# Performance work log

Hardware: AMD Instinct MI355X
Metric: run time of the kernel (lower is better)

Reference implementation:

```python
import jax, jax.numpy as jnp
import numpy as np

N_AUTHORS = 50000
N_PAPERS = 100000
N_NODES = N_AUTHORS + N_PAPERS
N_EDGES = 1200000
EMB_DIM = 64
NUM_LAYERS = 3


def setup_inputs() -> dict:
    key = jax.random.key(0)
    k1, k2, k3, k4, k5 = jax.random.split(key, 5)
    author_embedding = jax.random.normal(k1, (N_AUTHORS, EMB_DIM), dtype=jnp.float32)
    paper_embedding = jax.random.normal(k2, (N_PAPERS, EMB_DIM), dtype=jnp.float32)
    adj_rows = jax.random.randint(k3, (N_EDGES,), 0, N_NODES, dtype=jnp.int32)
    adj_cols = jax.random.randint(k4, (N_EDGES,), 0, N_NODES, dtype=jnp.int32)
    # symmetric-normalized adjacency values are small positive floats
    adj_vals = jax.random.uniform(k5, (N_EDGES,), dtype=jnp.float32) * 0.1
    return {
        "author_embedding": author_embedding,
        "paper_embedding": paper_embedding,
        "adj_rows": adj_rows,
        "adj_cols": adj_cols,
        "adj_vals": adj_vals,
    }


def _spmm(adj_rows, adj_cols, adj_vals, x):
    # sparse [N,N] @ dense [N,d] via gather + segment_sum
    msgs = adj_vals[:, None] * x[adj_cols]  # [E, d]
    return jax.ops.segment_sum(msgs, adj_rows, num_segments=N_NODES)


def reference(author_embedding, paper_embedding, adj_rows, adj_cols, adj_vals):
    ego = jnp.concatenate([author_embedding, paper_embedding], axis=0)  # [N, d]
    acc = ego
    x = ego
    for _ in range(NUM_LAYERS):
        x = _spmm(adj_rows, adj_cols, adj_vals, x)
        acc = acc + x
    out = acc / jnp.float32(NUM_LAYERS + 1)  # mean over layer outputs
    out_author = out[:N_AUTHORS]
    out_paper = out[N_AUTHORS:]
    return ego, out_author, out_paper
```

## Files before the change

kernel.cpp:

```cpp
#include <hip/hip_runtime.h>

#define N_AUTHORS 50000
#define N_PAPERS  100000
#define N_NODES   150000
#define N_EDGES   1200000
#define EMB       64

#define BSHIFT 10
#define K_B    ((N_NODES + 1023) >> 10)
#define CHUNK  4096
#define NBLK_A ((N_EDGES + CHUNK - 1) / CHUNK)
#define NSC    (K_B * NBLK_A)
#define NBS1   ((NSC + 1023) / 1024)

typedef float v2f __attribute__((ext_vector_type(2)));

__device__ __forceinline__ ushort f2bf(float f) {
    unsigned u = __float_as_uint(f);
    return (ushort)((u + 0x7fffu + ((u >> 16) & 1u)) >> 16);
}
#define bfLO(u) __uint_as_float((u) << 16)
#define bfHI(u) __uint_as_float((u) & 0xffff0000u)

__device__ __forceinline__ v2f mkv2(float a, float b) { v2f r; r.x = a; r.y = b; return r; }
__device__ __forceinline__ v2f bfv2(unsigned u) { return mkv2(bfLO(u), bfHI(u)); }

__device__ __forceinline__ v2f red_v2(v2f v) {
#pragma unroll
    for (int s = 8; s <= 32; s <<= 1) {
        v2f o;
        o.x = __shfl_xor(v.x, s, 64);
        o.y = __shfl_xor(v.y, s, 64);
        v += o;
    }
    return v;
}

__global__ void lgcn_hist_init(const int* __restrict__ rows,
                               unsigned* __restrict__ counts,
                               const float* __restrict__ a,
                               const float* __restrict__ p,
                               float* __restrict__ ego_out,
                               ushort* __restrict__ x0) {
    __shared__ unsigned h[K_B];
    int t = threadIdx.x;
    if (blockIdx.x < NBLK_A) {
        for (int i = t; i < K_B; i += blockDim.x) h[i] = 0;
        __syncthreads();
        int base = blockIdx.x * CHUNK;
        int end  = base + CHUNK; if (end > N_EDGES) end = N_EDGES;
        for (int e = base + t; e < end; e += blockDim.x)
            atomicAdd(&h[rows[e] >> BSHIFT], 1u);
        __syncthreads();
        for (int i = t; i < K_B; i += blockDim.x)
            counts[(size_t)i * NBLK_A + blockIdx.x] = h[i];
    } else {
        size_t i = (size_t)(blockIdx.x - NBLK_A) * blockDim.x + t;
        const size_t n4  = (size_t)N_NODES  * EMB / 4;
        const size_t au4 = (size_t)N_AUTHORS * EMB / 4;
        if (i >= n4) return;
        float4 v = (i < au4) ? ((const float4*)a)[i] : ((const float4*)p)[i - au4];
        ((float4*)ego_out)[i] = v;
        ushort4 b;
        b.x = f2bf(v.x); b.y = f2bf(v.y); b.z = f2bf(v.z); b.w = f2bf(v.w);
        ((ushort4*)x0)[i] = b;
    }
}

__global__ void lgcn_scan_l1(const unsigned* __restrict__ counts,
                             unsigned* __restrict__ scanned,
                             unsigned* __restrict__ btot) {
    __shared__ unsigned s[1024];
    int t = threadIdx.x;
    int i = blockIdx.x * 1024 + t;
    unsigned v = (i < NSC) ? counts[i] : 0u;
    s[t] = v;
    __syncthreads();
    for (int d = 1; d < 1024; d <<= 1) {
        unsigned u = (t >= d) ? s[t - d] : 0u;
        __syncthreads();
        s[t] += u;
        __syncthreads();
    }
    if (i < NSC) scanned[i] = s[t] - v;
    if (t == 1023) btot[blockIdx.x] = s[1023];
}

__device__ __forceinline__ void btot_prefix(const unsigned* __restrict__ btot,
                                            unsigned* __restrict__ btex) {
    if (threadIdx.x == 0) {
        unsigned run = 0;
        for (int i = 0; i < NBS1; ++i) { btex[i] = run; run += btot[i]; }
    }
    __syncthreads();
}

__global__ void lgcn_a1_bin(const int* __restrict__ rows,
                            const int* __restrict__ cols,
                            const float* __restrict__ vals,
                            const unsigned* __restrict__ scanned,
                            const unsigned* __restrict__ btot,
                            float2* __restrict__ stage) {
    __shared__ unsigned cur[K_B];
    __shared__ unsigned btex[NBS1];
    btot_prefix(btot, btex);
    int t = threadIdx.x;
    for (int i = t; i < K_B; i += blockDim.x) {
        unsigned idx = (unsigned)i * NBLK_A + blockIdx.x;
        cur[i] = scanned[idx] + btex[idx >> 10];
    }
    __syncthreads();
    int base = blockIdx.x * CHUNK;
    int end  = base + CHUNK; if (end > N_EDGES) end = N_EDGES;
    for (int e = base + t; e < end; e += blockDim.x) {
        int r = rows[e];
        unsigned pos = atomicAdd(&cur[r >> BSHIFT], 1u);
        unsigned packed = ((unsigned)(r & 1023) << 18) | (unsigned)cols[e];
        stage[pos] = make_float2(__uint_as_float(packed), vals[e]);
    }
}

__global__ void lgcn_place(const unsigned* __restrict__ scanned,
                           const unsigned* __restrict__ btot,
                           const float2* __restrict__ stage,
                           float2* __restrict__ se,
                           unsigned* __restrict__ row_start) {
    __shared__ unsigned cur[1 << BSHIFT];
    __shared__ unsigned tsum[256];
    __shared__ unsigned btex[NBS1];
    btot_prefix(btot, btex);
    int b  = blockIdx.x;
    int rb = b << BSHIFT;
    int nrows = N_NODES - rb; if (nrows > (1 << BSHIFT)) nrows = 1 << BSHIFT;
    int t = threadIdx.x;

    unsigned i0 = (unsigned)b * NBLK_A;
    unsigned base = scanned[i0] + btex[i0 >> 10];
    unsigned span1;
    if (b + 1 < K_B) {
        unsigned i1 = (unsigned)(b + 1) * NBLK_A;
        span1 = scanned[i1] + btex[i1 >> 10];
    } else span1 = N_EDGES;

    for (int i = t; i < (1 << BSHIFT); i += 256) cur[i] = 0;
    __syncthreads();
    for (unsigned p = base + t; p < span1; p += 256)
        atomicAdd(&cur[__float_as_uint(stage[p].x) >> 18], 1u);
    __syncthreads();

    unsigned c[4], s = 0;
#pragma unroll
    for (int k = 0; k < 4; ++k) { c[k] = cur[t * 4 + k]; s += c[k]; }
    tsum[t] = s;
    __syncthreads();
    for (int d = 1; d < 256; d <<= 1) {
        unsigned u = (t >= d) ? tsum[t - d] : 0u;
        __syncthreads();
        tsum[t] += u;
        __syncthreads();
    }
    unsigned run = base + (tsum[t] - s);
    __syncthreads();
#pragma unroll
    for (int k = 0; k < 4; ++k) {
        int i = t * 4 + k;
        cur[i] = run;
        if (i < nrows) row_start[rb + i] = run;
        run += c[k];
    }
    if (b == K_B - 1 && t == 0) row_start[N_NODES] = N_EDGES;
    __syncthreads();

    for (unsigned p = base + t; p < span1; p += 256) {
        float2 v = stage[p];
        unsigned u = __float_as_uint(v.x);
        unsigned pos = atomicAdd(&cur[u >> 18], 1u);
        se[pos] = make_float2(__int_as_float((int)(u & 0x3FFFFu)), v.y);
    }
}

template <int MODE>
__global__ void lgcn_spmm(const unsigned* __restrict__ rs,
                          const float2* __restrict__ se,
                          const ushort* __restrict__ xb,
                          const unsigned char* __restrict__ x8,
                          unsigned char* __restrict__ y8,
                          const ushort* __restrict__ egob,
                          const unsigned char* __restrict__ y18,
                          float* __restrict__ out) {
    int w    = blockIdx.x * (blockDim.x >> 6) + (threadIdx.x >> 6);
    int lane = threadIdx.x & 63;
    int r0   = w << 1;
    if (r0 >= N_NODES) return;
    unsigned jA   = rs[r0];
    unsigned endA = rs[r0 + 1];
    unsigned jB   = endA;
    unsigned endB = rs[r0 + 2];
    const int g  = lane >> 3;
    const int d8 = (lane & 7) << 3;
    v2f A0 = {0.f, 0.f}, A1 = A0, A2 = A0, A3 = A0;
    v2f B0 = A0, B1 = A0, B2 = A0, B3 = A0;

#define BATCH8(JB, END, P0, P1, P2, P3)                                       \
    {                                                                         \
        unsigned idx = (JB) + g;                                              \
        float2 e;                                                             \
        if (idx < (END)) e = se[idx];                                         \
        else { e.x = __int_as_float(0); e.y = 0.f; }                          \
        v2f ey = mkv2(e.y, e.y);                                              \
        if constexpr (MODE == 0) {                                            \
            const uint4 xv = *(const uint4*)(xb + ((size_t)__float_as_int(e.x) << 6) + d8); \
            P0 += ey * bfv2(xv.x);                                            \
            P1 += ey * bfv2(xv.y);                                            \
            P2 += ey * bfv2(xv.z);                                            \
            P3 += ey * bfv2(xv.w);                                            \
        } else {                                                              \
            const uint2 xv = *(const uint2*)(x8 + ((size_t)__float_as_int(e.x) << 6) + d8); \
            P0 += ey * __builtin_amdgcn_cvt_pk_f32_fp8((int)xv.x, false);     \
            P1 += ey * __builtin_amdgcn_cvt_pk_f32_fp8((int)xv.x, true);      \
            P2 += ey * __builtin_amdgcn_cvt_pk_f32_fp8((int)xv.y, false);     \
            P3 += ey * __builtin_amdgcn_cvt_pk_f32_fp8((int)xv.y, true);      \
        }                                                                     \
    }

    BATCH8(jA, endA, A0, A1, A2, A3)
    BATCH8(jB, endB, B0, B1, B2, B3)
    jA += 8; jB += 8;
    while (jA < endA) { BATCH8(jA, endA, A0, A1, A2, A3) jA += 8; }
    while (jB < endB) { BATCH8(jB, endB, B0, B1, B2, B3) jB += 8; }
#undef BATCH8

    A0 = red_v2(A0); A1 = red_v2(A1); A2 = red_v2(A2); A3 = red_v2(A3);
    B0 = red_v2(B0); B1 = red_v2(B1); B2 = red_v2(B2); B3 = red_v2(B3);

    if (g == 0) {
#define EMIT(ROW, P0, P1, P2, P3)                                             \
    {                                                                         \
        size_t o = ((size_t)(ROW) << 6) + d8;                                 \
        if constexpr (MODE == 2) {                                            \
            uint4 ue = *(const uint4*)(egob + o);                             \
            uint2 u1 = *(const uint2*)(y18 + o);                              \
            uint2 u2 = *(const uint2*)(x8 + o);                               \
            v2f q = mkv2(0.25f, 0.25f);                                       \
            v2f r0 = (bfv2(ue.x) + __builtin_amdgcn_cvt_pk_f32_fp8((int)u1.x, false) \
                      + __builtin_amdgcn_cvt_pk_f32_fp8((int)u2.x, false) + P0) * q; \
            v2f r1 = (bfv2(ue.y) + __builtin_amdgcn_cvt_pk_f32_fp8((int)u1.x, true)  \
                      + __builtin_amdgcn_cvt_pk_f32_fp8((int)u2.x, true) + P1) * q; \
            v2f r2 = (bfv2(ue.z) + __builtin_amdgcn_cvt_pk_f32_fp8((int)u1.y, false) \
                      + __builtin_amdgcn_cvt_pk_f32_fp8((int)u2.y, false) + P2) * q; \
            v2f r3 = (bfv2(ue.w) + __builtin_amdgcn_cvt_pk_f32_fp8((int)u1.y, true)  \
                      + __builtin_amdgcn_cvt_pk_f32_fp8((int)u2.y, true) + P3) * q; \
            float4 lo, hi;                                                    \
            lo.x = r0.x; lo.y = r0.y; lo.z = r1.x; lo.w = r1.y;               \
            hi.x = r2.x; hi.y = r2.y; hi.z = r3.x; hi.w = r3.y;               \
            *(float4*)(out + o)     = lo;                                     \
            *(float4*)(out + o + 4) = hi;                                     \
        } else {                                                              \
            int w0 = __builtin_amdgcn_cvt_pk_fp8_f32(P0.x, P0.y, 0, false);   \
            w0     = __builtin_amdgcn_cvt_pk_fp8_f32(P1.x, P1.y, w0, true);   \
            int w1 = __builtin_amdgcn_cvt_pk_fp8_f32(P2.x, P2.y, 0, false);   \
            w1     = __builtin_amdgcn_cvt_pk_fp8_f32(P3.x, P3.y, w1, true);   \
            uint2 ov8; ov8.x = (unsigned)w0; ov8.y = (unsigned)w1;            \
            *(uint2*)(y8 + o) = ov8;                                          \
        }                                                                     \
    }
        EMIT(r0, A0, A1, A2, A3)
        EMIT(r0 + 1, B0, B1, B2, B3)
#undef EMIT
    }
}

extern "C" void kernel_launch(void* const* d_in, const int* in_sizes, int n_in,
                              void* d_out, int out_size, void* d_ws, size_t ws_size,
                              hipStream_t stream) {
    const float* author = (const float*)d_in[0];
    const float* paper  = (const float*)d_in[1];
    const int*   rows   = (const int*)d_in[2];
    const int*   cols   = (const int*)d_in[3];
    const float* vals   = (const float*)d_in[4];

    float* ego_out = (float*)d_out;
    float* acc     = (float*)d_out + (size_t)N_NODES * EMB;

    char* w = (char*)d_ws;
    float2*   se        = (float2*)w;   w += (size_t)N_EDGES * sizeof(float2);
    float2*   stage     = (float2*)w;   w += (size_t)N_EDGES * sizeof(float2);
    ushort*   xbE       = (ushort*)w;   w += (size_t)N_NODES * EMB * sizeof(ushort);
    unsigned char* y2_8 = (unsigned char*)w; w += (size_t)N_NODES * EMB;
    unsigned* row_start = (unsigned*)w; w += (size_t)(N_NODES + 1) * 4;
    unsigned* bcounts   = (unsigned*)w; w += (size_t)NSC * 4;
    unsigned* bscanned  = (unsigned*)w; w += (size_t)NSC * 4;
    unsigned* btot      = (unsigned*)w; w += 64 * 4;
    unsigned char* y1_8 = (unsigned char*)stage;

    const int BLK = 256;
    const int g_vec  = (int)(((size_t)N_NODES * EMB / 4 + BLK - 1) / BLK);
    const int g_spmm = ((N_NODES / 2) + 3) / 4;

    lgcn_hist_init<<<NBLK_A + g_vec, BLK, 0, stream>>>(rows, bcounts,
                                                       author, paper, ego_out, xbE);

    lgcn_scan_l1<<<NBS1, 1024, 0, stream>>>(bcounts, bscanned, btot);

    lgcn_a1_bin<<<NBLK_A, BLK, 0, stream>>>(rows, cols, vals, bscanned, btot, stage);
    lgcn_place<<<K_B, BLK, 0, stream>>>(bscanned, btot, stage, se, row_start);

    lgcn_spmm<0><<<g_spmm, BLK, 0, stream>>>(row_start, se, xbE, nullptr,
                                             y1_8, nullptr, nullptr, nullptr);
    lgcn_spmm<1><<<g_spmm, BLK, 0, stream>>>(row_start, se, nullptr, y1_8,
                                             y2_8, nullptr, nullptr, nullptr);
    lgcn_spmm<2><<<g_spmm, BLK, 0, stream>>>(row_start, se, nullptr, y2_8,
                                             nullptr, xbE, y1_8, acc);
}
```

Measured before the change: 191.9 us.

## Split each SpMM layer into two column-range passes for gather locality

Each row's edges are now sorted into two halves by source column (below or above 75000), and row_mid marks the boundary. Each SpMM layer then runs as two passes, one per column half, so the gathered source features of each pass fit better in L2/MALL. The first pass writes a bf16 partial result that the second pass reads back and adds. This costs an extra launch per layer and an extra round trip of the partial buffer, and it adds one bf16 rounding step.

```diff
diff --git a/kernel.cpp b/kernel.cpp
--- a/kernel.cpp
+++ b/kernel.cpp
@@ -5,6 +5,7 @@
 #define N_NODES   150000
 #define N_EDGES   1200000
 #define EMB       64
+#define COL_SPLIT 75000u
 
 #define BSHIFT 10
 #define K_B    ((N_NODES + 1023) >> 10)
@@ -124,8 +125,9 @@
                            const unsigned* __restrict__ btot,
                            const float2* __restrict__ stage,
                            float2* __restrict__ se,
-                           unsigned* __restrict__ row_start) {
-    __shared__ unsigned cur[1 << BSHIFT];
+                           unsigned* __restrict__ row_start,
+                           unsigned* __restrict__ row_mid) {
+    __shared__ unsigned cur[2048];
     __shared__ unsigned tsum[256];
     __shared__ unsigned btex[NBS1];
     btot_prefix(btot, btex);
@@ -142,15 +144,18 @@
         span1 = scanned[i1] + btex[i1 >> 10];
     } else span1 = N_EDGES;
 
-    for (int i = t; i < (1 << BSHIFT); i += 256) cur[i] = 0;
-    __syncthreads();
-    for (unsigned p = base + t; p < span1; p += 256)
-        atomicAdd(&cur[__float_as_uint(stage[p].x) >> 18], 1u);
-    __syncthreads();
-
-    unsigned c[4], s = 0;
+    for (int i = t; i < 2048; i += 256) cur[i] = 0;
+    __syncthreads();
+    for (unsigned p = base + t; p < span1; p += 256) {
+        unsigned u = __float_as_uint(stage[p].x);
+        unsigned bin = ((u >> 18) << 1) | ((u & 0x3FFFFu) >= COL_SPLIT ? 1u : 0u);
+        atomicAdd(&cur[bin], 1u);
+    }
+    __syncthreads();
+
+    unsigned c[8], s = 0;
 #pragma unroll
-    for (int k = 0; k < 4; ++k) { c[k] = cur[t * 4 + k]; s += c[k]; }
+    for (int k = 0; k < 8; ++k) { c[k] = cur[t * 8 + k]; s += c[k]; }
     tsum[t] = s;
     __syncthreads();
     for (int d = 1; d < 256; d <<= 1) {
@@ -162,10 +167,14 @@
     unsigned run = base + (tsum[t] - s);
     __syncthreads();
 #pragma unroll
-    for (int k = 0; k < 4; ++k) {
-        int i = t * 4 + k;
-        cur[i] = run;
-        if (i < nrows) row_start[rb + i] = run;
+    for (int k = 0; k < 8; ++k) {
+        int bin = t * 8 + k;
+        cur[bin] = run;
+        int row = bin >> 1;
+        if (row < nrows) {
+            if ((bin & 1) == 0) row_start[rb + row] = run;
+            else                row_mid[rb + row]   = run;
+        }
         run += c[k];
     }
     if (b == K_B - 1 && t == 0) row_start[N_NODES] = N_EDGES;
@@ -174,16 +183,20 @@
     for (unsigned p = base + t; p < span1; p += 256) {
         float2 v = stage[p];
         unsigned u = __float_as_uint(v.x);
-        unsigned pos = atomicAdd(&cur[u >> 18], 1u);
-        se[pos] = make_float2(__int_as_float((int)(u & 0x3FFFFu)), v.y);
-    }
-}
-
-template <int MODE>
+        unsigned col = u & 0x3FFFFu;
+        unsigned bin = ((u >> 18) << 1) | (col >= COL_SPLIT ? 1u : 0u);
+        unsigned pos = atomicAdd(&cur[bin], 1u);
+        se[pos] = make_float2(__int_as_float((int)col), v.y);
+    }
+}
+
+template <int MODE, int PASS>
 __global__ void lgcn_spmm(const unsigned* __restrict__ rs,
+                          const unsigned* __restrict__ rmid,
                           const float2* __restrict__ se,
                           const ushort* __restrict__ xb,
                           const unsigned char* __restrict__ x8,
+                          ushort* __restrict__ yp,
                           unsigned char* __restrict__ y8,
                           const ushort* __restrict__ egob,
                           const unsigned char* __restrict__ y18,
@@ -192,10 +205,14 @@
     int lane = threadIdx.x & 63;
     int r0   = w << 1;
     if (r0 >= N_NODES) return;
-    unsigned jA   = rs[r0];
-    unsigned endA = rs[r0 + 1];
-    unsigned jB   = endA;
-    unsigned endB = rs[r0 + 2];
+    unsigned jA, endA, jB, endB;
+    if constexpr (PASS == 0) {
+        jA = rs[r0];       endA = rmid[r0];
+        jB = rs[r0 + 1];   endB = rmid[r0 + 1];
+    } else {
+        jA = rmid[r0];     endA = rs[r0 + 1];
+        jB = rmid[r0 + 1]; endB = rs[r0 + 2];
+    }
     const int g  = lane >> 3;
     const int d8 = (lane & 7) << 3;
     v2f A0 = {0.f, 0.f}, A1 = A0, A2 = A0, A3 = A0;
@@ -237,31 +254,43 @@
 #define EMIT(ROW, P0, P1, P2, P3)                                             \
     {                                                                         \
         size_t o = ((size_t)(ROW) << 6) + d8;                                 \
-        if constexpr (MODE == 2) {                                            \
-            uint4 ue = *(const uint4*)(egob + o);                             \
-            uint2 u1 = *(const uint2*)(y18 + o);                              \
-            uint2 u2 = *(const uint2*)(x8 + o);                               \
-            v2f q = mkv2(0.25f, 0.25f);                                       \
-            v2f r0 = (bfv2(ue.x) + __builtin_amdgcn_cvt_pk_f32_fp8((int)u1.x, false) \
-                      + __builtin_amdgcn_cvt_pk_f32_fp8((int)u2.x, false) + P0) * q; \
-            v2f r1 = (bfv2(ue.y) + __builtin_amdgcn_cvt_pk_f32_fp8((int)u1.x, true)  \
-                      + __builtin_amdgcn_cvt_pk_f32_fp8((int)u2.x, true) + P1) * q; \
-            v2f r2 = (bfv2(ue.z) + __builtin_amdgcn_cvt_pk_f32_fp8((int)u1.y, false) \
-                      + __builtin_amdgcn_cvt_pk_f32_fp8((int)u2.y, false) + P2) * q; \
-            v2f r3 = (bfv2(ue.w) + __builtin_amdgcn_cvt_pk_f32_fp8((int)u1.y, true)  \
-                      + __builtin_amdgcn_cvt_pk_f32_fp8((int)u2.y, true) + P3) * q; \
-            float4 lo, hi;                                                    \
-            lo.x = r0.x; lo.y = r0.y; lo.z = r1.x; lo.w = r1.y;               \
-            hi.x = r2.x; hi.y = r2.y; hi.z = r3.x; hi.w = r3.y;               \
-            *(float4*)(out + o)     = lo;                                     \
-            *(float4*)(out + o + 4) = hi;                                     \
+        if constexpr (PASS == 0) {                                            \
+            uint4 ov;                                                         \
+            ov.x = (unsigned)f2bf(P0.x) | ((unsigned)f2bf(P0.y) << 16);       \
+            ov.y = (unsigned)f2bf(P1.x) | ((unsigned)f2bf(P1.y) << 16);       \
+            ov.z = (unsigned)f2bf(P2.x) | ((unsigned)f2bf(P2.y) << 16);       \
+            ov.w = (unsigned)f2bf(P3.x) | ((unsigned)f2bf(P3.y) << 16);       \
+            *(uint4*)(yp + o) = ov;                                           \
         } else {                                                              \
-            int w0 = __builtin_amdgcn_cvt_pk_fp8_f32(P0.x, P0.y, 0, false);   \
-            w0     = __builtin_amdgcn_cvt_pk_fp8_f32(P1.x, P1.y, w0, true);   \
-            int w1 = __builtin_amdgcn_cvt_pk_fp8_f32(P2.x, P2.y, 0, false);   \
-            w1     = __builtin_amdgcn_cvt_pk_fp8_f32(P3.x, P3.y, w1, true);   \
-            uint2 ov8; ov8.x = (unsigned)w0; ov8.y = (unsigned)w1;            \
-            *(uint2*)(y8 + o) = ov8;                                          \
+            uint4 pv = *(const uint4*)(yp + o);                               \
+            P0 += bfv2(pv.x); P1 += bfv2(pv.y);                               \
+            P2 += bfv2(pv.z); P3 += bfv2(pv.w);                               \
+            if constexpr (MODE == 2) {                                        \
+                uint4 ue = *(const uint4*)(egob + o);                         \
+                uint2 u1 = *(const uint2*)(y18 + o);                          \
+                uint2 u2 = *(const uint2*)(x8 + o);                           \
+                v2f q = mkv2(0.25f, 0.25f);                                   \
+                v2f r0v = (bfv2(ue.x) + __builtin_amdgcn_cvt_pk_f32_fp8((int)u1.x, false) \
+                          + __builtin_amdgcn_cvt_pk_f32_fp8((int)u2.x, false) + P0) * q; \
+                v2f r1v = (bfv2(ue.y) + __builtin_amdgcn_cvt_pk_f32_fp8((int)u1.x, true)  \
+                          + __builtin_amdgcn_cvt_pk_f32_fp8((int)u2.x, true) + P1) * q; \
+                v2f r2v = (bfv2(ue.z) + __builtin_amdgcn_cvt_pk_f32_fp8((int)u1.y, false) \
+                          + __builtin_amdgcn_cvt_pk_f32_fp8((int)u2.y, false) + P2) * q; \
+                v2f r3v = (bfv2(ue.w) + __builtin_amdgcn_cvt_pk_f32_fp8((int)u1.y, true)  \
+                          + __builtin_amdgcn_cvt_pk_f32_fp8((int)u2.y, true) + P3) * q; \
+                float4 lo, hi;                                                \
+                lo.x = r0v.x; lo.y = r0v.y; lo.z = r1v.x; lo.w = r1v.y;       \
+                hi.x = r2v.x; hi.y = r2v.y; hi.z = r3v.x; hi.w = r3v.y;       \
+                *(float4*)(out + o)     = lo;                                 \
+                *(float4*)(out + o + 4) = hi;                                 \
+            } else {                                                          \
+                int w0 = __builtin_amdgcn_cvt_pk_fp8_f32(P0.x, P0.y, 0, false); \
+                w0     = __builtin_amdgcn_cvt_pk_fp8_f32(P1.x, P1.y, w0, true); \
+                int w1 = __builtin_amdgcn_cvt_pk_fp8_f32(P2.x, P2.y, 0, false); \
+                w1     = __builtin_amdgcn_cvt_pk_fp8_f32(P3.x, P3.y, w1, true); \
+                uint2 ov8; ov8.x = (unsigned)w0; ov8.y = (unsigned)w1;        \
+                *(uint2*)(y8 + o) = ov8;                                      \
+            }                                                                 \
         }                                                                     \
     }
         EMIT(r0, A0, A1, A2, A3)
@@ -286,8 +315,10 @@
     float2*   se        = (float2*)w;   w += (size_t)N_EDGES * sizeof(float2);
     float2*   stage     = (float2*)w;   w += (size_t)N_EDGES * sizeof(float2);
     ushort*   xbE       = (ushort*)w;   w += (size_t)N_NODES * EMB * sizeof(ushort);
+    ushort*   yp        = (ushort*)w;   w += (size_t)N_NODES * EMB * sizeof(ushort);
     unsigned char* y2_8 = (unsigned char*)w; w += (size_t)N_NODES * EMB;
     unsigned* row_start = (unsigned*)w; w += (size_t)(N_NODES + 1) * 4;
+    unsigned* row_mid   = (unsigned*)w; w += (size_t)N_NODES * 4;
     unsigned* bcounts   = (unsigned*)w; w += (size_t)NSC * 4;
     unsigned* bscanned  = (unsigned*)w; w += (size_t)NSC * 4;
     unsigned* btot      = (unsigned*)w; w += 64 * 4;
@@ -303,12 +334,18 @@
     lgcn_scan_l1<<<NBS1, 1024, 0, stream>>>(bcounts, bscanned, btot);
 
     lgcn_a1_bin<<<NBLK_A, BLK, 0, stream>>>(rows, cols, vals, bscanned, btot, stage);
-    lgcn_place<<<K_B, BLK, 0, stream>>>(bscanned, btot, stage, se, row_start);
-
-    lgcn_spmm<0><<<g_spmm, BLK, 0, stream>>>(row_start, se, xbE, nullptr,
-                                             y1_8, nullptr, nullptr, nullptr);
-    lgcn_spmm<1><<<g_spmm, BLK, 0, stream>>>(row_start, se, nullptr, y1_8,
-                                             y2_8, nullptr, nullptr, nullptr);
-    lgcn_spmm<2><<<g_spmm, BLK, 0, stream>>>(row_start, se, nullptr, y2_8,
-                                             nullptr, xbE, y1_8, acc);
-}
+    lgcn_place<<<K_B, BLK, 0, stream>>>(bscanned, btot, stage, se, row_start, row_mid);
+
+    lgcn_spmm<0, 0><<<g_spmm, BLK, 0, stream>>>(row_start, row_mid, se, xbE, nullptr,
+                                                yp, nullptr, nullptr, nullptr, nullptr);
+    lgcn_spmm<0, 1><<<g_spmm, BLK, 0, stream>>>(row_start, row_mid, se, xbE, nullptr,
+                                                yp, y1_8, nullptr, nullptr, nullptr);
+    lgcn_spmm<1, 0><<<g_spmm, BLK, 0, stream>>>(row_start, row_mid, se, nullptr, y1_8,
+                                                yp, nullptr, nullptr, nullptr, nullptr);
+    lgcn_spmm<1, 1><<<g_spmm, BLK, 0, stream>>>(row_start, row_mid, se, nullptr, y1_8,
+                                                yp, y2_8, nullptr, nullptr, nullptr);
+    lgcn_spmm<2, 0><<<g_spmm, BLK, 0, stream>>>(row_start, row_mid, se, nullptr, y2_8,
+                                                yp, nullptr, nullptr, nullptr, nullptr);
+    lgcn_spmm<2, 1><<<g_spmm, BLK, 0, stream>>>(row_start, row_mid, se, nullptr, y2_8,
+                                                yp, nullptr, xbE, y1_8, acc);
+}
```

Result: slower. 308.2 us (+60.6%).
